# Performance work log

Hardware: AMD Instinct MI355X
Metric: run time of the kernel (lower is better)

Reference implementation:

```python
import jax, jax.numpy as jnp
import numpy as np


def conv1d(x, w, b):
    # x: [B, C_in, T], w: [C_out, C_in, K] (torch layout), b: [C_out]
    y = jax.lax.conv_general_dilated(
        x, w, window_strides=(1,), padding='SAME',
        dimension_numbers=('NCH', 'OIH', 'NCH'))
    return y + b[None, :, None]


def setup_inputs() -> dict:
    B, T, IN, H, D, K = 16, 2048, 80, 512, 512, 1024
    key = jax.random.key(0)
    ks = jax.random.split(key, 10)
    f32 = jnp.float32

    def w_init(k, shape, fan_in):
        return (jax.random.normal(k, shape, f32) / np.sqrt(fan_in)).astype(f32)

    return {
        'mels':    jax.random.normal(ks[0], (B, T, IN), f32),
        'enc_w1':  w_init(ks[1], (H, IN, 3), IN * 3),
        'enc_b1':  jnp.zeros((H,), f32),
        'enc_w2':  w_init(ks[2], (D, H, 3), H * 3),
        'enc_b2':  jnp.zeros((D,), f32),
        'codebook': jax.random.normal(ks[3], (K, D), f32),
        'dec_w1':  w_init(ks[4], (H, D, 3), D * 3),
        'dec_b1':  jnp.zeros((H,), f32),
        'dec_w2':  w_init(ks[5], (IN, H, 3), H * 3),
        'dec_b2':  jnp.zeros((IN,), f32),
    }


def reference(mels, enc_w1, enc_b1, enc_w2, enc_b2, codebook,
              dec_w1, dec_b1, dec_w2, dec_b2):
    B, T, _ = mels.shape
    D = codebook.shape[1]

    # ---- encoder: conv -> relu -> conv ----
    x = jnp.swapaxes(mels, 1, 2)                      # [B, in_dim, T]
    z = conv1d(jax.nn.relu(conv1d(x, enc_w1, enc_b1)), enc_w2, enc_b2)  # [B, D, T]

    # ---- vector quantization ----
    z_t = jnp.swapaxes(z, 1, 2)                       # [B, T, D]
    flat = z_t.reshape(-1, D)                         # [B*T, D]
    d = ((flat ** 2).sum(axis=1, keepdims=True)
         - 2.0 * flat @ codebook.T
         + (codebook ** 2).sum(axis=1)[None, :])      # [B*T, K]
    idx = jnp.argmin(d, axis=1).reshape(B, T)         # [B, T] int
    quantized = codebook[idx]                         # [B, T, D] gather

    # ---- decoder: conv -> relu -> conv ----
    q = jnp.swapaxes(quantized, 1, 2)                 # [B, D, T]
    recon = conv1d(jax.nn.relu(conv1d(q, dec_w1, dec_b1)), dec_w2, dec_b2)
    recon = jnp.swapaxes(recon, 1, 2)                 # [B, T, in_dim]
    return recon, idx
```

## Files before the change

### kernel.cpp

```cpp
#include <hip/hip_runtime.h>
#include <hip/hip_bf16.h>

#define Bsz   16
#define Tn    2048
#define INC   80
#define Hc    512
#define Dc    512
#define NCODE 1024
#define BT    (Bsz * Tn)
#define RECON_N (Bsz * Tn * INC)
#define MARGIN 0.03f

typedef __attribute__((ext_vector_type(8))) short bf16x8;
typedef __attribute__((ext_vector_type(4))) float f32x4;
typedef __attribute__((ext_vector_type(4))) unsigned short u16x4;

static __device__ __forceinline__ unsigned short f2bf(float x) {
    unsigned u = __float_as_uint(x);
    u += 0x7FFF + ((u >> 16) & 1);
    return (unsigned short)(u >> 16);
}
static __device__ __forceinline__ float bf2f(unsigned short h) {
    return __uint_as_float((unsigned)h << 16);
}

typedef const __attribute__((address_space(1))) unsigned int* gas_p;
typedef __attribute__((address_space(3))) unsigned int* las_p;
static __device__ __forceinline__ void async16(const void* g, const void* l) {
    __builtin_amdgcn_global_load_lds(
        (gas_p)(unsigned long long)g,
        (las_p)(unsigned int)(unsigned long long)l,
        16, 0, 0);
}

__global__ __launch_bounds__(64)
void code_norms(const float* __restrict__ CB, float* __restrict__ CN) {
    int j = blockIdx.x;
    int lane = threadIdx.x;
    const float4* row = (const float4*)(CB + (size_t)j * Dc);
    float s = 0.f;
    #pragma unroll
    for (int i = 0; i < 2; ++i) {
        float4 v = row[lane + i * 64];
        s = fmaf(v.x, v.x, s);
        s = fmaf(v.y, v.y, s);
        s = fmaf(v.z, v.z, s);
        s = fmaf(v.w, v.w, s);
    }
    #pragma unroll
    for (int off = 32; off > 0; off >>= 1) s += __shfl_down(s, off, 64);
    if (lane == 0) CN[j] = s;
}

__global__ __launch_bounds__(256)
void cb_transpose(const float* __restrict__ CB, float* __restrict__ CBt) {
    const int j0 = blockIdx.x * 64;
    const int d0 = blockIdx.y * 64;
    __shared__ float ts[64][65];
    const int tid = threadIdx.x;
    for (int i = tid; i < 4096; i += 256) {
        int r = i >> 6, c = i & 63;
        ts[r][c] = CB[(size_t)(j0 + r) * Dc + d0 + c];
    }
    __syncthreads();
    for (int i = tid; i < 4096; i += 256) {
        int r = i >> 6, c = i & 63;
        CBt[(size_t)(d0 + r) * NCODE + j0 + c] = ts[c][r];
    }
}

__global__ __launch_bounds__(256)
void mels_transpose(const float* __restrict__ M, float* __restrict__ MT) {
    const int t0 = blockIdx.x * 64;
    const int b  = blockIdx.y;
    __shared__ float ts[64][84];
    const int tid = threadIdx.x;
    #pragma unroll
    for (int it = 0; it < 5; ++it) {
        int i = tid + it * 256;
        int t = i / 20, c4 = i % 20;
        *(float4*)&ts[t][c4 * 4] =
            *(const float4*)&M[((size_t)b * Tn + t0 + t) * INC + c4 * 4];
    }
    __syncthreads();
    #pragma unroll
    for (int it = 0; it < 20; ++it) {
        int i = tid + it * 256;
        int c = i >> 6, t = i & 63;
        MT[((size_t)b * INC + c) * Tn + t0 + t] = ts[t][c];
    }
}

__global__ __launch_bounds__(256)
void wt_transpose(const float* __restrict__ W, float* __restrict__ Wt,
                  int Cin, int Cout) {
    const int o0 = blockIdx.x * 64;
    const int c0 = blockIdx.y * 16;
    __shared__ float ts[48][65];
    const int tid = threadIdx.x;
    for (int i = tid; i < 64 * 48; i += 256) {
        int o = i / 48, ck = i % 48;
        int oo = o0 + o;
        float v = 0.f;
        if (oo < Cout) v = W[(size_t)oo * Cin * 3 + c0 * 3 + ck];
        ts[ck][o] = v;
    }
    __syncthreads();
    for (int i = tid; i < 48 * 64; i += 256) {
        int o = i & 63, ck = i >> 6;
        int oo = o0 + o;
        if (oo < Cout) Wt[(size_t)(c0 * 3 + ck) * Cout + oo] = ts[ck][o];
    }
}

__global__ __launch_bounds__(256)
void wsplit(const float* __restrict__ W, unsigned short* __restrict__ Whl) {
    int o = blockIdx.x, k = blockIdx.y;
    #pragma unroll
    for (int it = 0; it < 2; ++it) {
        int c = threadIdx.x + it * 256;
        float v = W[((size_t)o * Hc + c) * 3 + k];
        unsigned short h = f2bf(v);
        size_t base = ((size_t)(k * Hc + o) * 16 + (c >> 5)) * 64 + (c & 31);
        Whl[base] = h;
        Whl[base + 32] = f2bf(v - bf2f(h));
    }
}

__global__ __launch_bounds__(256)
void wsplit80(const float* __restrict__ W, unsigned short* __restrict__ Wh) {
    int o = blockIdx.x, k = blockIdx.y;
    #pragma unroll
    for (int it = 0; it < 2; ++it) {
        int c = threadIdx.x + it * 256;
        Wh[((size_t)k * INC + o) * Hc + c] = f2bf(W[((size_t)o * Hc + c) * 3 + k]);
    }
}

__global__ __launch_bounds__(256)
void cbsplit(const float* __restrict__ CB, unsigned short* __restrict__ CBhl) {
    int j = blockIdx.x;
    #pragma unroll
    for (int it = 0; it < 2; ++it) {
        int d = threadIdx.x + it * 256;
        float v = CB[(size_t)j * Dc + d];
        unsigned short h = f2bf(v);
        size_t base = ((size_t)j * 16 + (d >> 5)) * 64 + (d & 31);
        CBhl[base] = h;
        CBhl[base + 32] = f2bf(v - bf2f(h));
    }
}

__global__ __launch_bounds__(256)
void conv_enc1(const float* __restrict__ X, const float* __restrict__ Wt,
               const float* __restrict__ bias, unsigned short* __restrict__ Yhl) {
    const int t0 = blockIdx.x * 64;
    const int o0 = blockIdx.y * 128;
    const int b  = blockIdx.z;
    union SharedU {
        struct { float Xs[16][72]; float Ws[48][132]; } a;
        float Ys[128][69];
    };
    __shared__ __align__(16) SharedU su;
    float (&Xs)[16][72]  = su.a.Xs;
    float (&Ws)[48][132] = su.a.Ws;
    const int tid = threadIdx.x;
    const int tx = tid & 15, ty = tid >> 4;
    float acc[8][4] = {};
    const float* Xb = X + (size_t)b * INC * Tn;

    for (int c0 = 0; c0 < INC; c0 += 16) {
        for (int i = tid; i < 16 * 66; i += 256) {
            int cc = i / 66, tt = i % 66;
            int t = t0 + tt - 1;
            float v = 0.f;
            if (t >= 0 && t < Tn) v = Xb[(size_t)(c0 + cc) * Tn + t];
            Xs[cc][tt] = v;
        }
        for (int i = tid; i < 48 * 128; i += 256) {
            int o = i & 127, ck = i >> 7;
            Ws[ck][o] = Wt[(size_t)(c0 * 3 + ck) * Hc + o0 + o];
        }
        __syncthreads();
        #pragma unroll
        for (int cc = 0; cc < 16; ++cc) {
            float4 xa = *(const float4*)&Xs[cc][tx * 4];
            float2 xb2 = *(const float2*)&Xs[cc][tx * 4 + 4];
            float xv[6] = {xa.x, xa.y, xa.z, xa.w, xb2.x, xb2.y};
            #pragma unroll
            for (int k = 0; k < 3; ++k) {
                float4 wa = *(const float4*)&Ws[cc * 3 + k][ty * 4];
                float4 wb = *(const float4*)&Ws[cc * 3 + k][64 + ty * 4];
                float wv[8] = {wa.x, wa.y, wa.z, wa.w, wb.x, wb.y, wb.z, wb.w};
                #pragma unroll
                for (int i8 = 0; i8 < 8; ++i8)
                    #pragma unroll
                    for (int j = 0; j < 4; ++j)
                        acc[i8][j] = fmaf(wv[i8], xv[k + j], acc[i8][j]);
            }
        }
        __syncthreads();
    }
    #pragma unroll
    for (int og = 0; og < 2; ++og)
        #pragma unroll
        for (int oi = 0; oi < 4; ++oi) {
            int ol = og * 64 + ty * 4 + oi;
            float bv = bias[o0 + ol];
            const int i8 = og * 4 + oi;
            #pragma unroll
            for (int j = 0; j < 4; ++j)
                su.Ys[ol][tx * 4 + j] = fmaxf(acc[i8][j] + bv, 0.f);
        }
    __syncthreads();
    #pragma unroll
    for (int it = 0; it < 8; ++it) {
        int i = tid + it * 256;
        int oq = i & 31, t = i >> 5;
        int o4 = o0 + oq * 4;
        u16x4 h, l;
        #pragma unroll
        for (int r = 0; r < 4; ++r) {
            float v = su.Ys[oq * 4 + r][t];
            unsigned short hh = f2bf(v);
            h[r] = hh;
            l[r] = f2bf(v - bf2f(hh));
        }
        size_t base = ((size_t)(b * (Tn + 2) + 1 + t0 + t) * 16 + (o4 >> 5)) * 64
                      + (o4 & 31);
        *(u16x4*)(Yhl + base) = h;
        *(u16x4*)(Yhl + base + 32) = l;
    }
}

__global__ __launch_bounds__(256)
void zero_guards(unsigned short* __restrict__ Yhl) {
    const int b = blockIdx.x;
    u16x4 z = {0, 0, 0, 0};
    size_t r0 = (size_t)(b * (Tn + 2)) * 1024;
    size_t r1 = (size_t)(b * (Tn + 2) + Tn + 1) * 1024;
    *(u16x4*)(Yhl + r0 + threadIdx.x * 4) = z;
    *(u16x4*)(Yhl + r1 + threadIdx.x * 4) = z;
}

__global__ __launch_bounds__(256)
void split_t(const float* __restrict__ X, unsigned short* __restrict__ Yhl,
             int rowStride, int rowOff) {
    const int t0 = blockIdx.x * 64;
    const int c0 = blockIdx.y * 64;
    const int b  = blockIdx.z;
    __shared__ __align__(16) float ts[64][68];
    const int tid = threadIdx.x;
    #pragma unroll
    for (int it = 0; it < 4; ++it) {
        int i = tid + it * 256;
        int cc = i >> 4, t4 = i & 15;
        float4 v = *(const float4*)&X[((size_t)b * Hc + c0 + cc) * Tn + t0 + t4 * 4];
        ts[t4 * 4 + 0][cc] = v.x;
        ts[t4 * 4 + 1][cc] = v.y;
        ts[t4 * 4 + 2][cc] = v.z;
        ts[t4 * 4 + 3][cc] = v.w;
    }
    __syncthreads();
    #pragma unroll
    for (int it = 0; it < 4; ++it) {
        int i = tid + it * 256;
        int t = i >> 4, c4 = i & 15;
        int c = c0 + c4 * 4;
        float4 v = *(const float4*)&ts[t][c4 * 4];
        float va[4] = {v.x, v.y, v.z, v.w};
        u16x4 h, l;
        #pragma unroll
        for (int r = 0; r < 4; ++r) {
            unsigned short hh = f2bf(va[r]);
            h[r] = hh;
            l[r] = f2bf(va[r] - bf2f(hh));
        }
        size_t base = ((size_t)(b * rowStride + rowOff + t0 + t) * 16 + (c >> 5)) * 64
                      + (c & 31);
        *(u16x4*)(Yhl + base) = h;
        *(u16x4*)(Yhl + base + 32) = l;
    }
}

__global__ __launch_bounds__(256)
void conv_mid_mfma(const unsigned short* __restrict__ Xhl,
                   const unsigned short* __restrict__ Whl,
                   const float* __restrict__ bias,
                   float* __restrict__ Y) {
    const int t0 = blockIdx.x * 128;
    const int o0 = blockIdx.y * 128;
    const int b  = blockIdx.z;
    __shared__ __align__(16) unsigned short XL[2][136 * 64];
    const int tid  = threadIdx.x;
    const int lane = tid & 63;
    const int wave = tid >> 6;
    const int wm = wave >> 1, wn = wave & 1;
    const int m16 = lane & 15;
    const int q = lane >> 4;
    const int lrow = lane >> 3;
    const int lchk = (lane & 7) ^ lrow;
    const unsigned short* Xb = Xhl + ((size_t)b * (Tn + 2) + t0) * 1024
                               + (size_t)lrow * 1024 + lchk * 8;

    f32x4 acc[4][4];
    #pragma unroll
    for (int mt = 0; mt < 4; ++mt)
        #pragma unroll
        for (int nt = 0; nt < 4; ++nt)
            acc[mt][nt] = (f32x4){0.f, 0.f, 0.f, 0.f};

    #pragma unroll
    for (int i = 0; i < 5; ++i) {
        int ii = wave + i * 4;
        if (ii < 17)
            async16(Xb + (size_t)ii * 8192, &XL[0][ii * 512]);
    }

    for (int c0 = 0; c0 < Hc; c0 += 32) {
        const int buf = (c0 >> 5) & 1;
        __syncthreads();
        if (c0 + 32 < Hc) {
            const unsigned short* src = Xb + (size_t)((c0 >> 5) + 1) * 64;
            #pragma unroll
            for (int i = 0; i < 5; ++i) {
                int ii = wave + i * 4;
                if (ii < 17)
                    async16(src + (size_t)ii * 8192, &XL[buf ^ 1][ii * 512]);
            }
        }
        #pragma unroll
        for (int k = 0; k < 3; ++k) {
            bf16x8 Ah[4], Al[4];
            #pragma unroll
            for (int mt = 0; mt < 4; ++mt) {
                int o = o0 + wm * 64 + mt * 16 + m16;
                size_t base = ((size_t)(k * Hc + o) * 16 + (c0 >> 5)) * 64 + q * 8;
                Ah[mt] = *(const bf16x8*)(Whl + base);
                Al[mt] = *(const bf16x8*)(Whl + base + 32);
            }
            #pragma unroll
            for (int nt = 0; nt < 4; ++nt) {
                int row = wn * 64 + nt * 16 + m16 + k;
                const unsigned short* rp = &XL[buf][row * 64];
                int ph = (q ^ (row & 7)) * 8;
                union { bf16x8 v; uint4 u; } bh, bl;
                bh.u = *(const uint4*)(rp + ph);
                bl.u = *(const uint4*)(rp + (ph ^ 32));
                __builtin_amdgcn_s_setprio(1);
                #pragma unroll
                for (int mt = 0; mt < 4; ++mt)
                    acc[mt][nt] = __builtin_amdgcn_mfma_f32_16x16x32_bf16(
                        Ah[mt], bh.v, acc[mt][nt], 0, 0, 0);
                #pragma unroll
                for (int mt = 0; mt < 4; ++mt)
                    acc[mt][nt] = __builtin_amdgcn_mfma_f32_16x16x32_bf16(
                        Al[mt], bh.v, acc[mt][nt], 0, 0, 0);
                #pragma unroll
                for (int mt = 0; mt < 4; ++mt)
                    acc[mt][nt] = __builtin_amdgcn_mfma_f32_16x16x32_bf16(
                        Ah[mt], bl.v, acc[mt][nt], 0, 0, 0);
                __builtin_amdgcn_s_setprio(0);
            }
        }
    }
    float* Yb = Y + (size_t)b * Hc * Tn;
    #pragma unroll
    for (int mt = 0; mt < 4; ++mt) {
        int ob = o0 + wm * 64 + mt * 16 + q * 4;
        float4 bq = *(const float4*)&bias[ob];
        float bqa[4] = {bq.x, bq.y, bq.z, bq.w};
        #pragma unroll
        for (int nt = 0; nt < 4; ++nt) {
            int t = t0 + wn * 64 + nt * 16 + m16;
            #pragma unroll
            for (int r = 0; r < 4; ++r)
                Yb[(size_t)(ob + r) * Tn + t] = acc[mt][nt][r] + bqa[r];
        }
    }
}

__global__ __launch_bounds__(256)
void dec2_mfma(const float* __restrict__ X,
               const unsigned short* __restrict__ Wh2,
               const float* __restrict__ bias, float* __restrict__ OUT) {
    const int t0 = blockIdx.x * 128;
    const int b  = blockIdx.z;
    __shared__ unsigned short Xs[2][130 * 36];
    const int tid = threadIdx.x;
    const int lane = tid & 63;
    const int wn = tid >> 6;
    const int m16 = lane & 15;
    const int q = lane >> 4;
    const float* Xb = X + (size_t)b * Hc * Tn;

    f32x4 acc[5][2];
    #pragma unroll
    for (int mt = 0; mt < 5; ++mt)
        #pragma unroll
        for (int nt = 0; nt < 2; ++nt)
            acc[mt][nt] = (f32x4){0.f, 0.f, 0.f, 0.f};

    float xr[17];
    #pragma unroll
    for (int it = 0; it < 17; ++it) {
        int f = tid + it * 256;
        if (it < 16 || tid < 64) {
            int cc = f / 130, tt = f - cc * 130;
            int t = t0 + tt - 1;
            xr[it] = (t >= 0 && t < Tn) ? Xb[(size_t)cc * Tn + t] : 0.f;
        }
    }

    for (int c0 = 0; c0 < Hc; c0 += 32) {
        const int buf = (c0 >> 5) & 1;
        #pragma unroll
        for (int it = 0; it < 17; ++it) {
            int f = tid + it * 256;
            if (it < 16 || tid < 64) {
                int cc = f / 130, tt = f - cc * 130;
                Xs[buf][tt * 36 + cc] = f2bf(xr[it]);
            }
        }
        __syncthreads();
        if (c0 + 32 < Hc) {
            const float* Xc = Xb + (size_t)(c0 + 32) * Tn;
            #pragma unroll
            for (int it = 0; it < 17; ++it) {
                int f = tid + it * 256;
                if (it < 16 || tid < 64) {
                    int cc = f / 130, tt = f - cc * 130;
                    int t = t0 + tt - 1;
                    xr[it] = (t >= 0 && t < Tn) ? Xc[(size_t)cc * Tn + t] : 0.f;
                }
            }
        }
        #pragma unroll
        for (int k = 0; k < 3; ++k) {
            bf16x8 Ah[5];
            #pragma unroll
            for (int mt = 0; mt < 5; ++mt) {
                int o = mt * 16 + m16;
                Ah[mt] = *(const bf16x8*)(Wh2 + ((size_t)(k * INC + o)) * Hc + c0 + q * 8);
            }
            #pragma unroll
            for (int nt = 0; nt < 2; ++nt) {
                int tt = wn * 32 + nt * 16 + m16 + k;
                union { bf16x8 v; uint2 h[2]; } bh;
                const unsigned short* ph = Xs[buf] + tt * 36 + q * 8;
                bh.h[0] = *(const uint2*)ph; bh.h[1] = *(const uint2*)(ph + 4);
                #pragma unroll
                for (int mt = 0; mt < 5; ++mt)
                    acc[mt][nt] = __builtin_amdgcn_mfma_f32_16x16x32_bf16(
                        Ah[mt], bh.v, acc[mt][nt], 0, 0, 0);
            }
        }
    }
    #pragma unroll
    for (int mt = 0; mt < 5; ++mt) {
        float4 bq = *(const float4*)&bias[mt * 16 + q * 4];
        #pragma unroll
        for (int nt = 0; nt < 2; ++nt) {
            int t = t0 + wn * 32 + nt * 16 + m16;
            float4 r;
            r.x = acc[mt][nt][0] + bq.x;
            r.y = acc[mt][nt][1] + bq.y;
            r.z = acc[mt][nt][2] + bq.z;
            r.w = acc[mt][nt][3] + bq.w;
            *(float4*)(OUT + ((size_t)b * Tn + t) * INC + mt * 16 + q * 4) = r;
        }
    }
}

__global__ __launch_bounds__(256)
void vq_mfma(const unsigned short* __restrict__ Zt,
             const unsigned short* __restrict__ CBhl,
             const float* __restrict__ CN,
             float* __restrict__ candv, int* __restrict__ candi,
             float* __restrict__ cand2v) {
    const int nb = blockIdx.x;
    const int jb = blockIdx.y;
    const int b  = nb >> 4;
    const int t0 = (nb & 15) * 128;
    const int jbase = jb * 128;
    __shared__ __align__(16) unsigned char pool[32768];
    unsigned short* XL0 = (unsigned short*)pool;
    unsigned short* XL1 = (unsigned short*)(pool + 16384);
    float* RV = (float*)pool;
    int*   RI = (int*)(pool + 4096);
    float* R2 = (float*)(pool + 8192);

    const int tid = threadIdx.x;
    const int lane = tid & 63;
    const int wave = tid >> 6;
    const int wm = wave >> 1, wn = wave & 1;
    const int m16 = lane & 15;
    const int q = lane >> 4;
    const int lrow = lane >> 3;
    const int lchk = (lane & 7) ^ lrow;
    const unsigned short* Zb = Zt + (size_t)(b * Tn + t0) * 1024
                               + (size_t)lrow * 1024 + lchk * 8;

    f32x4 acc[4][4];
    #pragma unroll
    for (int mt = 0; mt < 4; ++mt)
        #pragma unroll
        for (int nt = 0; nt < 4; ++nt)
            acc[mt][nt] = (f32x4){0.f, 0.f, 0.f, 0.f};

    #pragma unroll
    for (int i = 0; i < 4; ++i) {
        int ii = wave + i * 4;
        async16(Zb + (size_t)ii * 8192, XL0 + ii * 512);
    }

    for (int d0 = 0; d0 < Dc; d0 += 32) {
        const int buf = (d0 >> 5) & 1;
        unsigned short* XL = buf ? XL1 : XL0;
        __syncthreads();
        if (d0 + 32 < Dc) {
            unsigned short* XN = buf ? XL0 : XL1;
            const unsigned short* src = Zb + (size_t)((d0 >> 5) + 1) * 64;
            #pragma unroll
            for (int i = 0; i < 4; ++i) {
                int ii = wave + i * 4;
                async16(src + (size_t)ii * 8192, XN + ii * 512);
            }
        }
        bf16x8 Ah[4], Al[4];
        #pragma unroll
        for (int mt = 0; mt < 4; ++mt) {
            int j = jbase + wm * 64 + mt * 16 + m16;
            size_t base = ((size_t)j * 16 + (d0 >> 5)) * 64 + q * 8;
            Ah[mt] = *(const bf16x8*)(CBhl + base);
            Al[mt] = *(const bf16x8*)(CBhl + base + 32);
        }
        #pragma unroll
        for (int nt = 0; nt < 4; ++nt) {
            int row = wn * 64 + nt * 16 + m16;
            const unsigned short* rp = XL + row * 64;
            int ph = (q ^ (row & 7)) * 8;
            union { bf16x8 v; uint4 u; } bh, bl;
            bh.u = *(const uint4*)(rp + ph);
            bl.u = *(const uint4*)(rp + (ph ^ 32));
            __builtin_amdgcn_s_setprio(1);
            #pragma unroll
            for (int mt = 0; mt < 4; ++mt)
                acc[mt][nt] = __builtin_amdgcn_mfma_f32_16x16x32_bf16(
                    Ah[mt], bh.v, acc[mt][nt], 0, 0, 0);
            #pragma unroll
            for (int mt = 0; mt < 4; ++mt)
                acc[mt][nt] = __builtin_amdgcn_mfma_f32_16x16x32_bf16(
                    Al[mt], bh.v, acc[mt][nt], 0, 0, 0);
            #pragma unroll
            for (int mt = 0; mt < 4; ++mt)
                acc[mt][nt] = __builtin_amdgcn_mfma_f32_16x16x32_bf16(
                    Ah[mt], bl.v, acc[mt][nt], 0, 0, 0);
            __builtin_amdgcn_s_setprio(0);
        }
    }
    __syncthreads();

    float cn4[4][4];
    #pragma unroll
    for (int mt = 0; mt < 4; ++mt) {
        float4 c = *(const float4*)&CN[jbase + wm * 64 + mt * 16 + q * 4];
        cn4[mt][0] = c.x; cn4[mt][1] = c.y; cn4[mt][2] = c.z; cn4[mt][3] = c.w;
    }
    #pragma unroll
    for (int nt = 0; nt < 4; ++nt) {
        int t = wn * 64 + nt * 16 + m16;
        float v1 = 1e30f, v2 = 1e30f;
        int i1 = 0;
        #pragma unroll
        for (int mt = 0; mt < 4; ++mt)
            #pragma unroll
            for (int r = 0; r < 4; ++r) {
                float d = fmaf(-2.f, acc[mt][nt][r], cn4[mt][r]);
                int j = jbase + wm * 64 + mt * 16 + q * 4 + r;
                if (d < v1 || (d == v1 && j < i1)) { v2 = v1; v1 = d; i1 = j; }
                else if (d < v2) v2 = d;
            }
        int slot = wm * 4 + q;
        RV[t * 8 + slot] = v1;
        RI[t * 8 + slot] = i1;
        R2[t * 8 + slot] = v2;
    }
    __syncthreads();
    if (tid < 128) {
        int t = tid;
        float v1 = RV[t * 8], v2 = R2[t * 8];
        int i1 = RI[t * 8];
        #pragma unroll
        for (int s = 1; s < 8; ++s) {
            float a1 = RV[t * 8 + s], a2 = R2[t * 8 + s];
            int ai = RI[t * 8 + s];
            if (a1 < v1 || (a1 == v1 && ai < i1)) {
                v2 = fminf(v1, a2); v1 = a1; i1 = ai;
            } else {
                v2 = fminf(v2, a1);
            }
        }
        int n = b * Tn + t0 + t;
        candv[(size_t)jb * BT + n] = v1;
        candi[(size_t)jb * BT + n] = i1;
        cand2v[(size_t)jb * BT + n] = v2;
    }
}

__global__ __launch_bounds__(256)
void vq_reduce2(const float* __restrict__ candv, const int* __restrict__ candi,
                const float* __restrict__ cand2v, int* __restrict__ idxI,
                float* __restrict__ idxf, int* __restrict__ flagn,
                int* __restrict__ flaglist) {
    int n = blockIdx.x * 256 + threadIdx.x;
    float v1 = candv[n], v2 = cand2v[n];
    int i1 = candi[n];
    #pragma unroll
    for (int jq = 1; jq < 8; ++jq) {
        float a1 = candv[(size_t)jq * BT + n];
        float a2 = cand2v[(size_t)jq * BT + n];
        int ai = candi[(size_t)jq * BT + n];
        if (a1 < v1 || (a1 == v1 && ai < i1)) {
            v2 = fminf(v1, a2); v1 = a1; i1 = ai;
        } else {
            v2 = fminf(v2, a1);
        }
    }
    idxI[n] = i1;
    idxf[n] = (float)i1;
    if (v2 - v1 < MARGIN) {
        int s = atomicAdd(flagn, 1);
        flaglist[s] = n;
    }
}

__global__ __launch_bounds__(256)
void vq_rescue(const int* __restrict__ flagn, const int* __restrict__ flaglist,
               const float* __restrict__ Z, const float* __restrict__ CB,
               const float* __restrict__ CN, int* __restrict__ idxI,
               float* __restrict__ idxf) {
    __shared__ float zs[512];
    __shared__ float rvv[256];
    __shared__ int   rii[256];
    const int nf = *flagn;
    for (int f = blockIdx.x; f < nf; f += gridDim.x) {
        int n = flaglist[f];
        int b = n / Tn, t = n - b * Tn;
        __syncthreads();
        #pragma unroll
        for (int it = 0; it < 2; ++it) {
            int d = threadIdx.x + it * 256;
            zs[d] = Z[((size_t)b * Dc + d) * Tn + t];
        }
        __syncthreads();
        float bv = 1e30f;
        int bi = 0;
        #pragma unroll
        for (int jj = 0; jj < 4; ++jj) {
            int j = threadIdx.x * 4 + jj;
            const float* cr = CB + (size_t)j * Dc;
            float dot = 0.f;
            for (int d = 0; d < Dc; ++d) dot = fmaf(zs[d], cr[d], dot);
            float dist = fmaf(-2.f, dot, CN[j]);
            if (dist < bv || (dist == bv && j < bi)) { bv = dist; bi = j; }
        }
        rvv[threadIdx.x] = bv;
        rii[threadIdx.x] = bi;
        __syncthreads();
        for (int off = 128; off > 0; off >>= 1) {
            if (threadIdx.x < off) {
                float ov = rvv[threadIdx.x + off];
                int oi = rii[threadIdx.x + off];
                if (ov < rvv[threadIdx.x] ||
                    (ov == rvv[threadIdx.x] && oi < rii[threadIdx.x])) {
                    rvv[threadIdx.x] = ov; rii[threadIdx.x] = oi;
                }
            }
            __syncthreads();
        }
        if (threadIdx.x == 0) {
            idxI[n] = rii[0];
            idxf[n] = (float)rii[0];
        }
    }
}

__global__ __launch_bounds__(256)
void gemm_g(const float* __restrict__ CBt, const float* __restrict__ Wt,
            float* __restrict__ G) {
    const int j0 = blockIdx.x * 64;
    const int kk = blockIdx.y >> 2;
    const int o0 = (blockIdx.y & 3) * 128;
    __shared__ __align__(16) float As[16][68];
    __shared__ __align__(16) float Bs[16][132];
    const int tid = threadIdx.x;
    const int tx = tid & 15, ty = tid >> 4;
    float acc[4][8] = {};

    for (int c0 = 0; c0 < Dc; c0 += 16) {
        {
            int cc = tid >> 4, j4 = tid & 15;
            *(float4*)&As[cc][j4 * 4] =
                *(const float4*)&CBt[(size_t)(c0 + cc) * NCODE + j0 + j4 * 4];
        }
        #pragma unroll
        for (int it = 0; it < 2; ++it) {
            int i = tid + it * 256;
            int cc = i >> 5, o4 = i & 31;
            *(float4*)&Bs[cc][o4 * 4] =
                *(const float4*)&Wt[(size_t)((c0 + cc) * 3 + kk) * Hc + o0 + o4 * 4];
        }
        __syncthreads();
        #pragma unroll
        for (int cc = 0; cc < 16; ++cc) {
            float4 a = *(const float4*)&As[cc][tx * 4];
            float av[4] = {a.x, a.y, a.z, a.w};
            float4 b0 = *(const float4*)&Bs[cc][ty * 4];
            float4 b1 = *(const float4*)&Bs[cc][64 + ty * 4];
            float bv[8] = {b0.x, b0.y, b0.z, b0.w, b1.x, b1.y, b1.z, b1.w};
            #pragma unroll
            for (int jj = 0; jj < 4; ++jj)
                #pragma unroll
                for (int oo = 0; oo < 8; ++oo)
                    acc[jj][oo] = fmaf(av[jj], bv[oo], acc[jj][oo]);
        }
        __syncthreads();
    }
    #pragma unroll
    for (int jj = 0; jj < 4; ++jj) {
        int j = j0 + tx * 4 + jj;
        float* gp = G + (size_t)j * 1536 + kk * 512 + o0;
        *(float4*)(gp + ty * 4) = *(float4*)&acc[jj][0];
        *(float4*)(gp + 64 + ty * 4) = *(float4*)&acc[jj][4];
    }
}

__global__ __launch_bounds__(256)
void dec_y3(const int* __restrict__ idx, const float* __restrict__ G,
            const float* __restrict__ bias, float* __restrict__ Y) {
    const int t0 = blockIdx.x * 64;
    const int o0 = blockIdx.y * 128;
    const int b  = blockIdx.z;
    const int tid = threadIdx.x;
    __shared__ int sidx[66];
    __shared__ __align__(16) float Ys[128][68];

    if (tid < 66) {
        int t = t0 + tid - 1;
        sidx[tid] = (t >= 0 && t < Tn) ? idx[b * Tn + t] : -1;
    }
    __syncthreads();

    const int o = tid & 127;
    const int half = tid >> 7;
    float acc[32] = {};
    #pragma unroll
    for (int kk = 0; kk < 3; ++kk) {
        const float* Gk = G + (size_t)kk * 512 + o0 + o;
        #pragma unroll
        for (int k = 0; k < 32; ++k) {
            int j = sidx[half + 2 * k + kk];
            if (j >= 0) acc[k] += Gk[(size_t)j * 1536];
        }
    }
    float bv = bias[o0 + o];
    #pragma unroll
    for (int k = 0; k < 32; ++k)
        Ys[o][half + 2 * k] = fmaxf(acc[k] + bv, 0.f);
    __syncthreads();

    float* Yb = Y + (size_t)b * Hc * Tn + t0;
    #pragma unroll
    for (int it = 0; it < 8; ++it) {
        int i = tid + it * 256;
        int t4 = i & 15, oo = i >> 4;
        *(float4*)&Yb[(size_t)(o0 + oo) * Tn + t4 * 4] =
            *(const float4*)&Ys[oo][t4 * 4];
    }
}

extern "C" void kernel_launch(void* const* d_in, const int* in_sizes, int n_in,
                              void* d_out, int out_size, void* d_ws, size_t ws_size,
                              hipStream_t stream) {
    const float* mels    = (const float*)d_in[0];
    const float* enc_w1  = (const float*)d_in[1];
    const float* enc_b1  = (const float*)d_in[2];
    const float* enc_w2  = (const float*)d_in[3];
    const float* enc_b2  = (const float*)d_in[4];
    const float* codebook= (const float*)d_in[5];
    const float* dec_w1  = (const float*)d_in[6];
    const float* dec_b1  = (const float*)d_in[7];
    const float* dec_w2  = (const float*)d_in[8];
    const float* dec_b2  = (const float*)d_in[9];

    float* out = (float*)d_out;
    float* recon = out;
    float* idxf  = out + RECON_N;

    const size_t ACT = (size_t)Bsz * Hc * Tn;
    const size_t Y1HL_U = (size_t)Bsz * (Tn + 2) * 1024 + 16384;
    const size_t R2F = Y1HL_U / 2;

    float* zf = (float*)d_ws;
    float* y3 = (float*)d_ws;
    float* r2 = (float*)d_ws + ACT;
    unsigned short* y1hl = (unsigned short*)r2;
    unsigned short* Zt   = (unsigned short*)r2;
    float* sm    = r2 + R2F;
    int*   idxI  = (int*)sm;
    float* cn    = (float*)(idxI + BT);
    float* cbt   = cn + NCODE;
    float* wt1   = cbt + (size_t)Dc * NCODE;
    float* wt3   = wt1 + (size_t)INC * 3 * Hc;
    float* candv = wt3 + (size_t)Dc * 3 * Hc;
    float* cand2v= candv + (size_t)8 * BT;
    int*   candi = (int*)(cand2v + (size_t)8 * BT);
    int*   flagn = candi + (size_t)8 * BT;
    int*   flaglist = flagn + 4;
    float* G     = (float*)(flaglist + BT);
    unsigned short* whl  = (unsigned short*)(G + (size_t)NCODE * 1536);
    unsigned short* cbhl = whl + (size_t)3 * Hc * 1024;
    unsigned short* wh2  = cbhl + (size_t)NCODE * 1024;
    float* melsT = (float*)(wh2 + (size_t)3 * INC * Hc);

    dim3 blk(256);
    hipMemsetAsync(flagn, 0, 16, stream);
    code_norms<<<dim3(NCODE), dim3(64), 0, stream>>>(codebook, cn);
    cb_transpose<<<dim3(NCODE / 64, Dc / 64), blk, 0, stream>>>(codebook, cbt);
    mels_transpose<<<dim3(Tn / 64, Bsz), blk, 0, stream>>>(mels, melsT);
    wt_transpose<<<dim3(Hc / 64, INC / 16), blk, 0, stream>>>(enc_w1, wt1, INC, Hc);
    wsplit<<<dim3(Hc, 3), blk, 0, stream>>>(enc_w2, whl);
    cbsplit<<<dim3(NCODE), blk, 0, stream>>>(codebook, cbhl);
    wt_transpose<<<dim3(Hc / 64, Dc / 16), blk, 0, stream>>>(dec_w1, wt3, Dc, Hc);
    wsplit80<<<dim3(INC, 3), blk, 0, stream>>>(dec_w2, wh2);
    gemm_g<<<dim3(NCODE / 64, 12), blk, 0, stream>>>(cbt, wt3, G);
    zero_guards<<<dim3(Bsz), blk, 0, stream>>>(y1hl);
    conv_enc1<<<dim3(Tn / 64, Hc / 128, Bsz), blk, 0, stream>>>(melsT, wt1, enc_b1,
                                                                y1hl);
    conv_mid_mfma<<<dim3(Tn / 128, Hc / 128, Bsz), blk, 0, stream>>>(y1hl, whl,
                                                                     enc_b2, zf);
    split_t<<<dim3(Tn / 64, Hc / 64, Bsz), blk, 0, stream>>>(zf, Zt, Tn, 0);
    vq_mfma<<<dim3(BT / 128, NCODE / 128), blk, 0, stream>>>(Zt, cbhl, cn,
                                                             candv, candi, cand2v);
    vq_reduce2<<<dim3(BT / 256), blk, 0, stream>>>(candv, candi, cand2v, idxI,
                                                   idxf, flagn, flaglist);
    vq_rescue<<<dim3(128), blk, 0, stream>>>(flagn, flaglist, zf, codebook, cn,
                                             idxI, idxf);
    dec_y3<<<dim3(Tn / 64, 4, Bsz), blk, 0, stream>>>(idxI, G, dec_b1, y3);
    dec2_mfma<<<dim3(Tn / 128, 1, Bsz), blk, 0, stream>>>(y3, wh2, dec_b2, recon);
}
```

Measured before the change: 803.2 us.

## Store decoder hidden as time-major bf16 and remap block order for L2 locality

dec_y3 now writes its ReLU output as bf16 in a time-major, zero-guarded layout, so dec2_mfma can stream tiles into swizzled LDS with async copies instead of loading strided fp32 and converting. This removes the fp32 write and read of the hidden activation and the per-element conversion. dec2 now works on 64-channel chunks with double buffering. Separately, conv_mid_mfma and vq_mfma remap block indices so that concurrently running blocks share inputs, aiming at better cache reuse. A small extra kernel zeroes the guard rows.

```diff
diff --git a/kernel.cpp b/kernel.cpp
--- a/kernel.cpp
+++ b/kernel.cpp
@@ -244,6 +244,18 @@
 }
 
 __global__ __launch_bounds__(256)
+void zero_guards512(unsigned short* __restrict__ Y) {
+    const int b = blockIdx.x;
+    u16x4 z = {0, 0, 0, 0};
+    size_t r0 = (size_t)(b * (Tn + 2)) * 512;
+    size_t r1 = (size_t)(b * (Tn + 2) + Tn + 1) * 512;
+    if (threadIdx.x < 128) {
+        *(u16x4*)(Y + r0 + threadIdx.x * 4) = z;
+        *(u16x4*)(Y + r1 + threadIdx.x * 4) = z;
+    }
+}
+
+__global__ __launch_bounds__(256)
 void split_t(const float* __restrict__ X, unsigned short* __restrict__ Yhl,
              int rowStride, int rowOff) {
     const int t0 = blockIdx.x * 64;
@@ -288,9 +300,11 @@
                    const unsigned short* __restrict__ Whl,
                    const float* __restrict__ bias,
                    float* __restrict__ Y) {
-    const int t0 = blockIdx.x * 128;
-    const int o0 = blockIdx.y * 128;
-    const int b  = blockIdx.z;
+    const int lin  = blockIdx.x + (blockIdx.y << 4) + (blockIdx.z << 6);
+    const int slot = lin >> 3;
+    const int b  = ((lin & 7) << 1) | (slot >> 6);
+    const int t0 = ((slot & 63) >> 2) << 7;
+    const int o0 = (slot & 3) << 7;
     __shared__ __align__(16) unsigned short XL[2][136 * 64];
     const int tid  = threadIdx.x;
     const int lane = tid & 63;
@@ -381,18 +395,22 @@
 }
 
 __global__ __launch_bounds__(256)
-void dec2_mfma(const float* __restrict__ X,
+void dec2_mfma(const unsigned short* __restrict__ Xt,
                const unsigned short* __restrict__ Wh2,
                const float* __restrict__ bias, float* __restrict__ OUT) {
     const int t0 = blockIdx.x * 128;
     const int b  = blockIdx.z;
-    __shared__ unsigned short Xs[2][130 * 36];
+    __shared__ __align__(16) unsigned short XL[2][136 * 64];
     const int tid = threadIdx.x;
     const int lane = tid & 63;
-    const int wn = tid >> 6;
+    const int wave = tid >> 6;
+    const int wn = wave;
     const int m16 = lane & 15;
     const int q = lane >> 4;
-    const float* Xb = X + (size_t)b * Hc * Tn;
+    const int lrow = lane >> 3;
+    const int lchk = (lane & 7) ^ lrow;
+    const unsigned short* Xb = Xt + ((size_t)b * (Tn + 2) + t0) * 512
+                               + (size_t)lrow * 512 + lchk * 8;
 
     f32x4 acc[5][2];
     #pragma unroll
@@ -401,58 +419,50 @@
         for (int nt = 0; nt < 2; ++nt)
             acc[mt][nt] = (f32x4){0.f, 0.f, 0.f, 0.f};
 
-    float xr[17];
-    #pragma unroll
-    for (int it = 0; it < 17; ++it) {
-        int f = tid + it * 256;
-        if (it < 16 || tid < 64) {
-            int cc = f / 130, tt = f - cc * 130;
-            int t = t0 + tt - 1;
-            xr[it] = (t >= 0 && t < Tn) ? Xb[(size_t)cc * Tn + t] : 0.f;
-        }
-    }
-
-    for (int c0 = 0; c0 < Hc; c0 += 32) {
-        const int buf = (c0 >> 5) & 1;
-        #pragma unroll
-        for (int it = 0; it < 17; ++it) {
-            int f = tid + it * 256;
-            if (it < 16 || tid < 64) {
-                int cc = f / 130, tt = f - cc * 130;
-                Xs[buf][tt * 36 + cc] = f2bf(xr[it]);
-            }
-        }
-        __syncthreads();
-        if (c0 + 32 < Hc) {
-            const float* Xc = Xb + (size_t)(c0 + 32) * Tn;
-            #pragma unroll
-            for (int it = 0; it < 17; ++it) {
-                int f = tid + it * 256;
-                if (it < 16 || tid < 64) {
-                    int cc = f / 130, tt = f - cc * 130;
-                    int t = t0 + tt - 1;
-                    xr[it] = (t >= 0 && t < Tn) ? Xc[(size_t)cc * Tn + t] : 0.f;
+    #pragma unroll
+    for (int i = 0; i < 5; ++i) {
+        int ii = wave + i * 4;
+        if (ii < 17)
+            async16(Xb + (size_t)ii * 4096, &XL[0][ii * 512]);
+    }
+
+    for (int c0 = 0; c0 < Hc; c0 += 64) {
+        const int buf = (c0 >> 6) & 1;
+        __syncthreads();
+        if (c0 + 64 < Hc) {
+            const unsigned short* src = Xb + (size_t)((c0 >> 6) + 1) * 64;
+            #pragma unroll
+            for (int i = 0; i < 5; ++i) {
+                int ii = wave + i * 4;
+                if (ii < 17)
+                    async16(src + (size_t)ii * 4096, &XL[buf ^ 1][ii * 512]);
+            }
+        }
+        #pragma unroll
+        for (int k = 0; k < 3; ++k) {
+            #pragma unroll
+            for (int sub = 0; sub < 2; ++sub) {
+                int c = c0 + sub * 32;
+                bf16x8 Ah[5];
+                #pragma unroll
+                for (int mt = 0; mt < 5; ++mt) {
+                    int o = mt * 16 + m16;
+                    Ah[mt] = *(const bf16x8*)(Wh2 + ((size_t)(k * INC + o)) * Hc
+                                              + c + q * 8);
                 }
-            }
-        }
-        #pragma unroll
-        for (int k = 0; k < 3; ++k) {
-            bf16x8 Ah[5];
-            #pragma unroll
-            for (int mt = 0; mt < 5; ++mt) {
-                int o = mt * 16 + m16;
-                Ah[mt] = *(const bf16x8*)(Wh2 + ((size_t)(k * INC + o)) * Hc + c0 + q * 8);
-            }
-            #pragma unroll
-            for (int nt = 0; nt < 2; ++nt) {
-                int tt = wn * 32 + nt * 16 + m16 + k;
-                union { bf16x8 v; uint2 h[2]; } bh;
-                const unsigned short* ph = Xs[buf] + tt * 36 + q * 8;
-                bh.h[0] = *(const uint2*)ph; bh.h[1] = *(const uint2*)(ph + 4);
                 #pragma unroll
-                for (int mt = 0; mt < 5; ++mt)
-                    acc[mt][nt] = __builtin_amdgcn_mfma_f32_16x16x32_bf16(
-                        Ah[mt], bh.v, acc[mt][nt], 0, 0, 0);
+                for (int nt = 0; nt < 2; ++nt) {
+                    int row = wn * 32 + nt * 16 + m16 + k;
+                    const unsigned short* rp = &XL[buf][row * 64];
+                    int p = sub * 4 + q;
+                    int ph = (p ^ (row & 7)) * 8;
+                    union { bf16x8 v; uint4 u; } bh;
+                    bh.u = *(const uint4*)(rp + ph);
+                    #pragma unroll
+                    for (int mt = 0; mt < 5; ++mt)
+                        acc[mt][nt] = __builtin_amdgcn_mfma_f32_16x16x32_bf16(
+                            Ah[mt], bh.v, acc[mt][nt], 0, 0, 0);
+                }
             }
         }
     }
@@ -478,8 +488,10 @@
              const float* __restrict__ CN,
              float* __restrict__ candv, int* __restrict__ candi,
              float* __restrict__ cand2v) {
-    const int nb = blockIdx.x;
-    const int jb = blockIdx.y;
+    const int lin  = blockIdx.x + (blockIdx.y << 8);
+    const int slotB = lin >> 3;
+    const int nb = ((lin & 7) << 5) | (slotB & 31);
+    const int jb = slotB >> 5;
     const int b  = nb >> 4;
     const int t0 = (nb & 15) * 128;
     const int jbase = jb * 128;
@@ -581,10 +593,10 @@
                 if (d < v1 || (d == v1 && j < i1)) { v2 = v1; v1 = d; i1 = j; }
                 else if (d < v2) v2 = d;
             }
-        int slot = wm * 4 + q;
-        RV[t * 8 + slot] = v1;
-        RI[t * 8 + slot] = i1;
-        R2[t * 8 + slot] = v2;
+        int slotw = wm * 4 + q;
+        RV[t * 8 + slotw] = v1;
+        RI[t * 8 + slotw] = i1;
+        R2[t * 8 + slotw] = v2;
     }
     __syncthreads();
     if (tid < 128) {
@@ -738,7 +750,7 @@
 
 __global__ __launch_bounds__(256)
 void dec_y3(const int* __restrict__ idx, const float* __restrict__ G,
-            const float* __restrict__ bias, float* __restrict__ Y) {
+            const float* __restrict__ bias, unsigned short* __restrict__ Yt) {
     const int t0 = blockIdx.x * 64;
     const int o0 = blockIdx.y * 128;
     const int b  = blockIdx.z;
@@ -770,13 +782,16 @@
         Ys[o][half + 2 * k] = fmaxf(acc[k] + bv, 0.f);
     __syncthreads();
 
-    float* Yb = Y + (size_t)b * Hc * Tn + t0;
+    unsigned short* Yb = Yt + ((size_t)(b * (Tn + 2) + 1 + t0)) * 512 + o0;
     #pragma unroll
     for (int it = 0; it < 8; ++it) {
         int i = tid + it * 256;
-        int t4 = i & 15, oo = i >> 4;
-        *(float4*)&Yb[(size_t)(o0 + oo) * Tn + t4 * 4] =
-            *(const float4*)&Ys[oo][t4 * 4];
+        int t = i >> 5, oq = i & 31;
+        u16x4 h;
+        #pragma unroll
+        for (int r = 0; r < 4; ++r)
+            h[r] = f2bf(Ys[oq * 4 + r][t]);
+        *(u16x4*)(Yb + (size_t)t * 512 + oq * 4) = h;
     }
 }
 
@@ -803,7 +818,7 @@
     const size_t R2F = Y1HL_U / 2;
 
     float* zf = (float*)d_ws;
-    float* y3 = (float*)d_ws;
+    unsigned short* y3t = (unsigned short*)d_ws;
     float* r2 = (float*)d_ws + ACT;
     unsigned short* y1hl = (unsigned short*)r2;
     unsigned short* Zt   = (unsigned short*)r2;
@@ -847,6 +862,7 @@
                                                    idxf, flagn, flaglist);
     vq_rescue<<<dim3(128), blk, 0, stream>>>(flagn, flaglist, zf, codebook, cn,
                                              idxI, idxf);
-    dec_y3<<<dim3(Tn / 64, 4, Bsz), blk, 0, stream>>>(idxI, G, dec_b1, y3);
-    dec2_mfma<<<dim3(Tn / 128, 1, Bsz), blk, 0, stream>>>(y3, wh2, dec_b2, recon);
-}
+    zero_guards512<<<dim3(Bsz), blk, 0, stream>>>(y3t);
+    dec_y3<<<dim3(Tn / 64, 4, Bsz), blk, 0, stream>>>(idxI, G, dec_b1, y3t);
+    dec2_mfma<<<dim3(Tn / 128, 1, Bsz), blk, 0, stream>>>(y3t, wh2, dec_b2, recon);
+}
```

Result: no change. 793.7 us (-1.2%).
